# Kernel tuning notes

Measured on AMD Instinct MI355X. Metric: run time of the kernel, lower is better.

The kernel has to match this reference:

```python
import jax, jax.numpy as jnp
import numpy as np

B, S, D = 1, 2048, 1024
H, HD = 16, 64            # attn_num, head dim (D = H*HD)
TE, K, ED = 16, 2, 512    # experts, top_k, expert_dim
DS = 2048                 # shared_expert_dim
EPS = 1e-5
THETA = 10000.0
RSF = 1.0                 # routed_scaling_factor


def rmsnorm(x, w):
    return x * jax.lax.rsqrt(jnp.mean(x * x, axis=-1, keepdims=True) + EPS) * w


def rope(x):
    # x: [B,H,S,a]; half-split rotary as in RotaryEmb
    a = x.shape[-1]
    inv = (1.0 / THETA) ** (jnp.arange(0, a, 2, dtype=jnp.float32) / a)
    fr = jnp.outer(jnp.arange(x.shape[2], dtype=jnp.float32), inv)[None, None]  # [1,1,S,a/2]
    c, s = jnp.cos(fr), jnp.sin(fr)
    x1, x2 = jnp.split(x, 2, axis=-1)
    return jnp.concatenate([x1 * c + x2 * s, -x1 * s + x2 * c], axis=-1)


def setup_inputs() -> dict:
    key = jax.random.key(0)
    ks = jax.random.split(key, 16)
    w = 0.02
    return {
        "x_input": jax.random.normal(ks[0], (B, S, D), jnp.float32),
        "indices": jax.random.randint(ks[1], (B * S, K), 0, TE),
        "values": jax.random.normal(ks[2], (B * S, K), jnp.float32),
        "attn_w": jax.random.normal(ks[3], (3 * D, D), jnp.float32) * w,
        "attn_o_w": jax.random.normal(ks[4], (D, D), jnp.float32) * w,
        "attn_norm_w": jnp.ones((D,), jnp.float32),
        "ffn_norm_w": jnp.ones((D,), jnp.float32),
        "ffn_experts": jax.random.normal(ks[5], (3, TE, D, ED), jnp.float32) * w,
        "main_keys": jax.random.normal(ks[6], (D, TE), jnp.float32) * w,
        "main_bias": jnp.zeros((TE,), jnp.float32),
        "output_coeff": jnp.ones((1, 1, D), jnp.float32),
        "ffn_up_w": jax.random.normal(ks[7], (2 * DS, D), jnp.float32) * w,
        "ffn_down_w": jax.random.normal(ks[8], (D, DS), jnp.float32) * w,
        "shared_norm_w": jnp.ones((D,), jnp.float32),
    }


def reference(x_input, indices, values, attn_w, attn_o_w, attn_norm_w, ffn_norm_w,
              ffn_experts, main_keys, main_bias, output_coeff, ffn_up_w,
              ffn_down_w, shared_norm_w):
    # --- attention block ---
    x = rmsnorm(x_input, attn_norm_w)
    qkv = x @ attn_w.T                                  # [B,S,3D]
    xq, xk, xv = jnp.split(qkv, 3, axis=-1)
    def heads(t):
        return t.reshape(B, S, H, HD).transpose(0, 2, 1, 3)  # [B,H,S,HD]
    q, k, v = rope(heads(xq)), rope(heads(xk)), heads(xv)
    att = jnp.einsum('bhqa,bhka->bhqk', q, k) / jnp.sqrt(jnp.float32(HD))
    causal = jnp.tril(jnp.ones((S, S), bool))
    att = jnp.where(causal, att, jnp.finfo(att.dtype).min)
    att = jax.nn.softmax(att, axis=-1)
    o = jnp.einsum('bhqk,bhka->bhqa', att, v)
    x_attn = o.transpose(0, 2, 1, 3).reshape(B, S, D)
    x_ffn_input = x_attn @ attn_o_w.T + x_input

    # --- router ---
    x_ffn = rmsnorm(x_ffn_input, ffn_norm_w)
    T = B * S
    token_values = (x_ffn @ main_keys).reshape(T, TE)
    tv = jnp.take_along_axis(token_values, indices, axis=-1)  # [T,K]
    vals = values + tv + main_bias[indices]
    scores = jax.nn.softmax(vals, axis=-1) * RSF              # [T,K]

    # --- grouped GEMM experts (SwiGLU), dense combine over experts ---
    combine = jnp.zeros((T, TE), x_ffn.dtype).at[
        jnp.arange(T)[:, None], indices].add(scores)          # [T,TE]
    xf = x_ffn.reshape(T, D)
    h1 = jnp.einsum('td,edh->eth', xf, ffn_experts[0])
    h2 = jnp.einsum('td,edh->eth', xf, ffn_experts[1])
    g = jax.nn.silu(h1) * h2                                  # [TE,T,ED]
    ye = jnp.einsum('eth,edh->etd', g, ffn_experts[2])        # [TE,T,D]
    y = jnp.einsum('etd,te->td', ye, combine).reshape(B, S, D)
    y = y * output_coeff

    # --- shared SwiGLU expert ---
    x1, x2 = jnp.split(x_ffn @ ffn_up_w.T, 2, axis=-1)
    y_shared = (jax.nn.silu(x1) * x2) @ ffn_down_w.T
    y_shared = rmsnorm(y_shared, shared_norm_w)

    return y + y_shared + x_ffn_input
```

## Files before the change

### kernel.cpp

```cpp
#include <hip/hip_runtime.h>
#include <hip/hip_bf16.h>

using bf16 = __hip_bfloat16;

#define S_   2048
#define D_   1024
#define H_   16
#define HD_  64
#define TE_  16
#define ED_  512
#define DS_  2048
#define CAP_ 512

#define NEG_ -1e30f

typedef __attribute__((ext_vector_type(8))) short bf16x8;
typedef __attribute__((ext_vector_type(4))) short bf16x4;
typedef __attribute__((ext_vector_type(4))) float f32x4;
#define MFMA16(a, b, c) __builtin_amdgcn_mfma_f32_16x16x32_bf16(a, b, c, 0, 0, 0)

__device__ __forceinline__ void storeF(float* p, float v) { *p = v; }
__device__ __forceinline__ void storeF(bf16* p, float v)  { *p = __float2bfloat16(v); }
__device__ __forceinline__ short cvt1(float f) {
    bf16 h = __float2bfloat16(f);
    return *(short*)&h;
}
__device__ __forceinline__ float b2f(short s) {
    return __uint_as_float(((unsigned)(unsigned short)s) << 16);
}

__device__ __forceinline__ void load16(const bf16* g, short* l) {
    __builtin_amdgcn_global_load_lds(
        (const __attribute__((address_space(1))) unsigned*)g,
        (__attribute__((address_space(3))) unsigned*)l, 16, 0, 0);
}

__global__ __launch_bounds__(256) void convert_kernel(
        const float* __restrict__ src, bf16* __restrict__ dst)
{
    const size_t i = ((size_t)blockIdx.x*256 + threadIdx.x)*8;
    const float4 f0 = *(const float4*)(src + i);
    const float4 f1 = *(const float4*)(src + i + 4);
    short t8[8];
    t8[0]=cvt1(f0.x); t8[1]=cvt1(f0.y); t8[2]=cvt1(f0.z); t8[3]=cvt1(f0.w);
    t8[4]=cvt1(f1.x); t8[5]=cvt1(f1.y); t8[6]=cvt1(f1.z); t8[7]=cvt1(f1.w);
    *(bf16x8*)(dst + i) = *(bf16x8*)t8;
}

__global__ __launch_bounds__(256) void mkT_kernel(
        const float* __restrict__ mk, float* __restrict__ mkT)
{
    const int idx = blockIdx.x*256 + threadIdx.x;
    const int e = idx >> 10, d = idx & 1023;
    mkT[idx] = mk[d*TE_ + e];
}

__global__ __launch_bounds__(256) void rmsnorm_kernel(
        const float* __restrict__ x, const float* __restrict__ w,
        bf16* __restrict__ out)
{
    const int t = blockIdx.x, tid = threadIdx.x;
    __shared__ float red[4];
    const float4 xv = *(const float4*)(x + (size_t)t*D_ + tid*4);
    float ss = xv.x*xv.x + xv.y*xv.y + xv.z*xv.z + xv.w*xv.w;
#pragma unroll
    for (int off = 32; off; off >>= 1) ss += __shfl_xor(ss, off, 64);
    if ((tid & 63) == 0) red[tid >> 6] = ss;
    __syncthreads();
    const float rn = rsqrtf((red[0]+red[1]+red[2]+red[3]) * (1.f/D_) + 1e-5f);
    const float4 wv = *(const float4*)(w + tid*4);
    short o[4];
    o[0] = cvt1(xv.x*rn*wv.x); o[1] = cvt1(xv.y*rn*wv.y);
    o[2] = cvt1(xv.z*rn*wv.z); o[3] = cvt1(xv.w*rn*wv.w);
    *(bf16x4*)(out + (size_t)t*D_ + tid*4) = *(bf16x4*)o;
}

template<typename OutT, bool HAS_RES, int BN>
__global__ __launch_bounds__(256) void gemm_mfma_bb_kernel(
    const bf16* __restrict__ A, const bf16* __restrict__ B,
    OutT* __restrict__ C, const float* __restrict__ Res,
    int M, int N, int K)
{
    constexpr int MI = (BN == 128) ? 4 : 2;
    __shared__ short As[2][128*32];
    __shared__ short Bs[2][BN*32];
    const int tid = threadIdx.x;
    const int w = tid >> 6, l = tid & 63;
    const int wm = (BN == 128) ? (w >> 1) : w;
    const int wn = (BN == 128) ? (w & 1) : 0;
    const int nwg = gridDim.x * gridDim.y;
    const int bid = blockIdx.y * gridDim.x + blockIdx.x;
    const int swz = ((nwg & 7) == 0) ? ((bid & 7) * (nwg >> 3) + (bid >> 3)) : bid;
    const int bx = swz % gridDim.x, by = swz / gridDim.x;
    const int m0 = by * 128, n0 = bx * BN;
    const int lr = l >> 2, lq = l & 3;
    const int fm = l & 15, fq = l >> 4;
    f32x4 acc[MI][4];
#pragma unroll
    for (int i = 0; i < MI; ++i)
#pragma unroll
        for (int j = 0; j < 4; ++j) acc[i][j] = (f32x4){0.f,0.f,0.f,0.f};

    const bf16* ga = A + (size_t)(m0 + w*16 + lr)*K + lq*8;
    const bf16* gb = B + (size_t)(n0 + w*16 + lr)*K + lq*8;
    load16(ga,                &As[0][(w*16)*32]);
    load16(ga + (size_t)64*K, &As[0][(64 + w*16)*32]);
    load16(gb,                &Bs[0][(w*16)*32]);
    if constexpr (BN == 128)
        load16(gb + (size_t)64*K, &Bs[0][(64 + w*16)*32]);
    __syncthreads();
    const int nk = K >> 5;
    for (int t = 0; t < nk; ++t) {
        const int cur = t & 1;
        if (t + 1 < nk) {
            const int k1 = (t + 1) << 5;
            load16(ga + k1,                &As[cur^1][(w*16)*32]);
            load16(ga + k1 + (size_t)64*K, &As[cur^1][(64 + w*16)*32]);
            load16(gb + k1,                &Bs[cur^1][(w*16)*32]);
            if constexpr (BN == 128)
                load16(gb + k1 + (size_t)64*K, &Bs[cur^1][(64 + w*16)*32]);
        }
        bf16x8 af[MI], bfr[4];
#pragma unroll
        for (int mi = 0; mi < MI; ++mi)
            af[mi] = *(const bf16x8*)&As[cur][(wm*(MI*16) + mi*16 + fm)*32 + fq*8];
#pragma unroll
        for (int ni = 0; ni < 4; ++ni)
            bfr[ni] = *(const bf16x8*)&Bs[cur][(wn*64 + ni*16 + fm)*32 + fq*8];
#pragma unroll
        for (int mi = 0; mi < MI; ++mi)
#pragma unroll
            for (int ni = 0; ni < 4; ++ni)
                acc[mi][ni] = MFMA16(af[mi], bfr[ni], acc[mi][ni]);
        __syncthreads();
    }
#pragma unroll
    for (int mi = 0; mi < MI; ++mi)
#pragma unroll
        for (int ni = 0; ni < 4; ++ni)
#pragma unroll
            for (int r = 0; r < 4; ++r) {
                const int row = m0 + wm*(MI*16) + mi*16 + fq*4 + r;
                const int col = n0 + wn*64 + ni*16 + fm;
                float v = acc[mi][ni][r];
                if constexpr (HAS_RES) v += Res[(size_t)row*N + col];
                storeF(&C[(size_t)row*N + col], v);
            }
}

__global__ __launch_bounds__(256) void transpose_kernel(
    const float* __restrict__ src, bf16* __restrict__ dst)
{
    __shared__ bf16 tile[64][65];
    const int h0 = blockIdx.x*64, d0 = blockIdx.y*64, m = blockIdx.z;
    const float* s = src + (size_t)m*D_*ED_;
    bf16*        o = dst + (size_t)m*ED_*D_;
    const int tid = threadIdx.x;
#pragma unroll
    for (int i = 0; i < 16; ++i) {
        const int idx = tid + 256*i;
        const int r = idx >> 6, c = idx & 63;
        tile[r][c] = __float2bfloat16(s[(size_t)(d0 + r)*ED_ + h0 + c]);
    }
    __syncthreads();
#pragma unroll
    for (int i = 0; i < 16; ++i) {
        const int idx = tid + 256*i;
        const int r = idx >> 6, c = idx & 63;
        o[(size_t)(h0 + r)*D_ + d0 + c] = tile[c][r];
    }
}

__global__ __launch_bounds__(256) void expert_mid_mfma_kernel(
    const bf16* __restrict__ xffn, const bf16* __restrict__ w0t,
    const int* __restrict__ counts, const int* __restrict__ pairs,
    const float* __restrict__ pw, bf16* __restrict__ gbuf)
{
    const int ht = blockIdx.x, pt = blockIdx.y, e = blockIdx.z;
    const int cnt = counts[e];
    if (pt*128 >= cnt) return;
    __shared__ short Xs[2][128*32];
    __shared__ short W0s[2][64*32];
    __shared__ short W1s[2][64*32];
    __shared__ int   toks[128];
    __shared__ float wrow[128];
    const int tid = threadIdx.x;
    const int w = tid >> 6, l = tid & 63;
    const int wm = w >> 1, wn = w & 1;
    const int lr = l >> 2, lq = l & 3;
    const int fm = l & 15, fq = l >> 4;
    if (tid < 128) {
        const int p = pt*128 + tid;
        if (p < cnt) { toks[tid] = pairs[e*CAP_ + p] >> 1; wrow[tid] = pw[e*CAP_ + p]; }
        else         { toks[tid] = 0;                      wrow[tid] = 0.f; }
    }
    __syncthreads();
    const int t0 = toks[w*16 + lr], t1 = toks[64 + w*16 + lr];
    const bf16* gx0 = xffn + (size_t)t0*D_ + lq*8;
    const bf16* gx1 = xffn + (size_t)t1*D_ + lq*8;
    const bf16* g0  = w0t + ((size_t)e*ED_ + ht*64 + w*16 + lr)*D_ + lq*8;
    const bf16* g1  = w0t + ((size_t)(16 + e)*ED_ + ht*64 + w*16 + lr)*D_ + lq*8;
    f32x4 acc1[4][2], acc2[4][2];
#pragma unroll
    for (int i = 0; i < 4; ++i)
#pragma unroll
        for (int j = 0; j < 2; ++j) {
            acc1[i][j] = (f32x4){0.f,0.f,0.f,0.f};
            acc2[i][j] = (f32x4){0.f,0.f,0.f,0.f};
        }
    load16(gx0, &Xs[0][(w*16)*32]);
    load16(gx1, &Xs[0][(64 + w*16)*32]);
    load16(g0,  &W0s[0][(w*16)*32]);
    load16(g1,  &W1s[0][(w*16)*32]);
    __syncthreads();
    const int nk = D_ >> 5;
    for (int t = 0; t < nk; ++t) {
        const int cur = t & 1;
        if (t + 1 < nk) {
            const int k1 = (t + 1) << 5;
            load16(gx0 + k1, &Xs[cur^1][(w*16)*32]);
            load16(gx1 + k1, &Xs[cur^1][(64 + w*16)*32]);
            load16(g0 + k1,  &W0s[cur^1][(w*16)*32]);
            load16(g1 + k1,  &W1s[cur^1][(w*16)*32]);
        }
        bf16x8 af[4], b0[2], b1[2];
#pragma unroll
        for (int mi = 0; mi < 4; ++mi)
            af[mi] = *(const bf16x8*)&Xs[cur][(wm*64 + mi*16 + fm)*32 + fq*8];
#pragma unroll
        for (int ni = 0; ni < 2; ++ni) {
            b0[ni] = *(const bf16x8*)&W0s[cur][(wn*32 + ni*16 + fm)*32 + fq*8];
            b1[ni] = *(const bf16x8*)&W1s[cur][(wn*32 + ni*16 + fm)*32 + fq*8];
        }
#pragma unroll
        for (int mi = 0; mi < 4; ++mi)
#pragma unroll
            for (int ni = 0; ni < 2; ++ni) {
                acc1[mi][ni] = MFMA16(af[mi], b0[ni], acc1[mi][ni]);
                acc2[mi][ni] = MFMA16(af[mi], b1[ni], acc2[mi][ni]);
            }
        __syncthreads();
    }
#pragma unroll
    for (int mi = 0; mi < 4; ++mi)
#pragma unroll
        for (int ni = 0; ni < 2; ++ni)
#pragma unroll
            for (int r = 0; r < 4; ++r) {
                const int row = wm*64 + mi*16 + fq*4 + r;
                const int col = wn*32 + ni*16 + fm;
                const float h1 = acc1[mi][ni][r], h2 = acc2[mi][ni][r];
                const float g = wrow[row] * (h1 / (1.f + __expf(-h1))) * h2;
                gbuf[((size_t)e*CAP_ + pt*128 + row)*ED_ + ht*64 + col] = __float2bfloat16(g);
            }
}

__global__ __launch_bounds__(256) void expert_down_mfma_kernel(
    const bf16* __restrict__ gbuf, const bf16* __restrict__ w2,
    const int* __restrict__ counts, const int* __restrict__ pairs,
    bf16* __restrict__ ytk)
{
    const int nt = blockIdx.x, pt = blockIdx.y, e = blockIdx.z;
    const int cnt = counts[e];
    if (pt*128 >= cnt) return;
    __shared__ short As[2][128*32];
    __shared__ short Bs[2][128*32];
    __shared__ int prs[128];
    const int tid = threadIdx.x;
    const int w = tid >> 6, l = tid & 63;
    const int wm = w >> 1, wn = w & 1;
    const int lr = l >> 2, lq = l & 3;
    const int fm = l & 15, fq = l >> 4;
    if (tid < 128) {
        const int p = pt*128 + tid;
        prs[tid] = (p < cnt) ? pairs[e*CAP_ + p] : -1;
    }
    __syncthreads();
    const bf16* ga = gbuf + ((size_t)e*CAP_ + pt*128 + w*16 + lr)*ED_ + lq*8;
    const bf16* gb = w2 + (size_t)e*D_*ED_ + (size_t)(nt*128 + w*16 + lr)*ED_ + lq*8;
    f32x4 acc[4][4];
#pragma unroll
    for (int i = 0; i < 4; ++i)
#pragma unroll
        for (int j = 0; j < 4; ++j) acc[i][j] = (f32x4){0.f,0.f,0.f,0.f};
    load16(ga,                  &As[0][(w*16)*32]);
    load16(ga + (size_t)64*ED_, &As[0][(64 + w*16)*32]);
    load16(gb,                  &Bs[0][(w*16)*32]);
    load16(gb + (size_t)64*ED_, &Bs[0][(64 + w*16)*32]);
    __syncthreads();
    const int nk = ED_ >> 5;
    for (int t = 0; t < nk; ++t) {
        const int cur = t & 1;
        if (t + 1 < nk) {
            const int k1 = (t + 1) << 5;
            load16(ga + k1,                  &As[cur^1][(w*16)*32]);
            load16(ga + k1 + (size_t)64*ED_, &As[cur^1][(64 + w*16)*32]);
            load16(gb + k1,                  &Bs[cur^1][(w*16)*32]);
            load16(gb + k1 + (size_t)64*ED_, &Bs[cur^1][(64 + w*16)*32]);
        }
        bf16x8 af[4], bfr[4];
#pragma unroll
        for (int mi = 0; mi < 4; ++mi)
            af[mi] = *(const bf16x8*)&As[cur][(wm*64 + mi*16 + fm)*32 + fq*8];
#pragma unroll
        for (int ni = 0; ni < 4; ++ni)
            bfr[ni] = *(const bf16x8*)&Bs[cur][(wn*64 + ni*16 + fm)*32 + fq*8];
#pragma unroll
        for (int mi = 0; mi < 4; ++mi)
#pragma unroll
            for (int ni = 0; ni < 4; ++ni)
                acc[mi][ni] = MFMA16(af[mi], bfr[ni], acc[mi][ni]);
        __syncthreads();
    }
#pragma unroll
    for (int mi = 0; mi < 4; ++mi)
#pragma unroll
        for (int r = 0; r < 4; ++r) {
            const int pr = prs[wm*64 + mi*16 + fq*4 + r];
            if (pr < 0) continue;
#pragma unroll
            for (int ni = 0; ni < 4; ++ni) {
                const int col = nt*128 + wn*64 + ni*16 + fm;
                ytk[(size_t)pr*D_ + col] = __float2bfloat16(acc[mi][ni][r]);
            }
        }
}

__global__ __launch_bounds__(256) void rope_kernel(const bf16* __restrict__ qkv,
        bf16* __restrict__ qr, bf16* __restrict__ kswz)
{
    const int s = blockIdx.x, tid = threadIdx.x;
    const int c = s & 63, jt = s >> 6;
    for (int it = tid; it < 512; it += 256) {
        const int h = it >> 5, i = it & 31;
        const float inv = exp2f(-(float)i * 0.41524101186091903f);
        const float fr = (float)s * inv;
        float sn, cs;
        sincosf(fr, &sn, &cs);
        const size_t qb = (size_t)s*3072 + h*64 + i;
        const float q1 = __bfloat162float(qkv[qb]);
        const float q2 = __bfloat162float(qkv[qb + 32]);
        const size_t ob = ((size_t)h*S_ + s)*64 + i;
        qr[ob]      = __float2bfloat16(0.125f*( q1*cs + q2*sn));
        qr[ob + 32] = __float2bfloat16(0.125f*(-q1*sn + q2*cs));
        const float k1 = __bfloat162float(qkv[qb + 1024]);
        const float k2 = __bfloat162float(qkv[qb + 1024 + 32]);
        const size_t kb = ((size_t)(h*32 + jt))*4096 + (size_t)c*64;
        const int j0 = (i >> 3) ^ (c & 7);
        const int j1 = (4 + (i >> 3)) ^ (c & 7);
        kswz[kb + j0*8 + (i & 7)] = __float2bfloat16( k1*cs + k2*sn);
        kswz[kb + j1*8 + (i & 7)] = __float2bfloat16(-k1*sn + k2*cs);
    }
}

__global__ __launch_bounds__(256) void vtrans_kernel(
    const bf16* __restrict__ qkv, bf16* __restrict__ vswz)
{
    const int jt = blockIdx.x, h = blockIdx.y;
    __shared__ short Vt[64][72];
    const int tid = threadIdx.x;
#pragma unroll
    for (int it = 0; it < 2; ++it) {
        const int idx = it*256 + tid;
        const int cc = idx >> 3, seg = idx & 7;
        *(bf16x8*)&Vt[cc][seg*8] =
            *(const bf16x8*)(qkv + (size_t)(jt*64 + cc)*3072 + 2048 + h*64 + seg*8);
    }
    __syncthreads();
    bf16* out = vswz + ((size_t)(h*32 + jt))*4096;
#pragma unroll
    for (int it = 0; it < 2; ++it) {
        const int q = it*256 + tid;
        const int a = q >> 3, jo = q & 7;
        const int j = jo ^ (a & 7);
        short t8[8];
#pragma unroll
        for (int e = 0; e < 8; ++e) t8[e] = Vt[j*8 + e][a];
        *(bf16x8*)(out + a*64 + jo*8) = *(bf16x8*)t8;
    }
}

__global__ __launch_bounds__(512) void attn_mfma_kernel(
    const bf16* __restrict__ qr, const bf16* __restrict__ kswz,
    const bf16* __restrict__ vswz, bf16* __restrict__ xattn)
{
    const int p = blockIdx.x, h = blockIdx.y;
    __shared__ short Ks[2][2][4096];
    __shared__ short Vs[2][2][4096];
    __shared__ short Ps[2][64][72];
    __shared__ float Oc[64][64];
    __shared__ float Mc[64], Lc[64];
    const int tid = threadIdx.x;
    const int w = tid >> 6, l = tid & 63;
    const int g = w >> 2, gw = w & 3;
    const int fm = l & 15, fq = l >> 4;
    const int sr = gw * 16;
    const bf16* ktile = kswz + (size_t)h*32*4096;
    const bf16* vtile = vswz + (size_t)h*32*4096;

    auto stageKV = [&](int jtile, int bufidx) {
        const bf16* ks_ = ktile + (size_t)jtile*4096 + gw*1024 + l*8;
        const bf16* vs_ = vtile + (size_t)jtile*4096 + gw*1024 + l*8;
        short* kd_ = &Ks[g][bufidx][gw*1024];
        short* vd_ = &Vs[g][bufidx][gw*1024];
        load16(ks_,       kd_);
        load16(ks_ + 512, kd_ + 512);
        load16(vs_,       vd_);
        load16(vs_ + 512, vd_ + 512);
    };

    for (int half = 0; half < 2; ++half) {
        const int qt = half ? (31 - p) : p;
        const bf16* gq = qr + ((size_t)h*S_ + qt*64 + sr + fm)*64 + fq*8;
        const bf16x8 aq0 = *(const bf16x8*)gq;
        const bf16x8 aq1 = *(const bf16x8*)(gq + 32);
        f32x4 Oa[4];
        float m_i[4], l_i[4];
#pragma unroll
        for (int i = 0; i < 4; ++i) {
            Oa[i] = (f32x4){0.f,0.f,0.f,0.f};
            m_i[i] = NEG_; l_i[i] = 0.f;
        }
        const int nj = qt + 1;
        const int itmax = (nj + 1) >> 1;
        if (g < nj) stageKV(g, 0);
        __syncthreads();
        for (int it = 0; it < itmax; ++it) {
            const int jt = g + 2*it;
            const int buf = it & 1;
            if (jt + 2 < nj) stageKV(jt + 2, buf ^ 1);
            if (jt < nj) {
                const short* kb = &Ks[g][buf][0];
                const short* vb = &Vs[g][buf][0];
                f32x4 sc[4];
#pragma unroll
                for (int ni = 0; ni < 4; ++ni) sc[ni] = (f32x4){0.f,0.f,0.f,0.f};
                __builtin_amdgcn_s_setprio(1);
#pragma unroll
                for (int ni = 0; ni < 4; ++ni) {
                    const int row = ni*16 + fm;
                    bf16x8 bk0 = *(const bf16x8*)&kb[row*64 + (( fq      ^ (fm & 7))<<3)];
                    bf16x8 bk1 = *(const bf16x8*)&kb[row*64 + (((fq + 4) ^ (fm & 7))<<3)];
                    sc[ni] = MFMA16(aq0, bk0, sc[ni]);
                    sc[ni] = MFMA16(aq1, bk1, sc[ni]);
                }
                __builtin_amdgcn_s_setprio(0);
                const bool diag = (jt == qt);
#pragma unroll
                for (int r = 0; r < 4; ++r) {
                    const int rowin = sr + fq*4 + r;
                    float rm = NEG_;
#pragma unroll
                    for (int ni = 0; ni < 4; ++ni) {
                        if (diag && (ni*16 + fm) > rowin) sc[ni][r] = NEG_;
                        rm = fmaxf(rm, sc[ni][r]);
                    }
                    rm = fmaxf(rm, __shfl_xor(rm, 1, 16));
                    rm = fmaxf(rm, __shfl_xor(rm, 2, 16));
                    rm = fmaxf(rm, __shfl_xor(rm, 4, 16));
                    rm = fmaxf(rm, __shfl_xor(rm, 8, 16));
                    const float mnew  = fmaxf(m_i[r], rm);
                    const float alpha = __expf(m_i[r] - mnew);
                    float rs = 0.f;
#pragma unroll
                    for (int ni = 0; ni < 4; ++ni) {
                        const float pv = __expf(sc[ni][r] - mnew);
                        sc[ni][r] = pv; rs += pv;
                    }
                    rs += __shfl_xor(rs, 1, 16);
                    rs += __shfl_xor(rs, 2, 16);
                    rs += __shfl_xor(rs, 4, 16);
                    rs += __shfl_xor(rs, 8, 16);
                    l_i[r] = l_i[r]*alpha + rs;
                    m_i[r] = mnew;
#pragma unroll
                    for (int ni = 0; ni < 4; ++ni) Oa[ni][r] *= alpha;
                }
#pragma unroll
                for (int ni = 0; ni < 4; ++ni)
#pragma unroll
                    for (int r = 0; r < 4; ++r)
                        Ps[g][sr + fq*4 + r][ni*16 + fm] = cvt1(sc[ni][r]);
                bf16x8 ap0 = *(const bf16x8*)&Ps[g][sr + fm][fq*8];
                bf16x8 ap1 = *(const bf16x8*)&Ps[g][sr + fm][32 + fq*8];
                __builtin_amdgcn_s_setprio(1);
#pragma unroll
                for (int ni = 0; ni < 4; ++ni) {
                    const int row = ni*16 + fm;
                    bf16x8 bv0 = *(const bf16x8*)&vb[row*64 + (( fq      ^ (fm & 7))<<3)];
                    bf16x8 bv1 = *(const bf16x8*)&vb[row*64 + (((fq + 4) ^ (fm & 7))<<3)];
                    Oa[ni] = MFMA16(ap0, bv0, Oa[ni]);
                    Oa[ni] = MFMA16(ap1, bv1, Oa[ni]);
                }
                __builtin_amdgcn_s_setprio(0);
            }
            __syncthreads();
        }
        if (g == 1) {
#pragma unroll
            for (int r = 0; r < 4; ++r) {
                const int row = sr + fq*4 + r;
                if (fm == 0) { Mc[row] = m_i[r]; Lc[row] = l_i[r]; }
#pragma unroll
                for (int ni = 0; ni < 4; ++ni) Oc[row][ni*16 + fm] = Oa[ni][r];
            }
        }
        __syncthreads();
        if (g == 0) {
#pragma unroll
            for (int r = 0; r < 4; ++r) {
                const int row = sr + fq*4 + r;
                const float m1 = Mc[row], l1 = Lc[row];
                const float mm = fmaxf(m_i[r], m1);
                const float a0 = __expf(m_i[r] - mm), a1 = __expf(m1 - mm);
                const float inv = 1.f / (l_i[r]*a0 + l1*a1);
                const int srow = qt*64 + row;
#pragma unroll
                for (int ni = 0; ni < 4; ++ni)
                    xattn[(size_t)srow*D_ + h*64 + ni*16 + fm] =
                        __float2bfloat16((Oa[ni][r]*a0 + Oc[row][ni*16 + fm]*a1)*inv);
            }
        }
        __syncthreads();
    }
}

__global__ __launch_bounds__(256) void router_kernel(
    const bf16* __restrict__ xffn, const int* __restrict__ indices,
    const float* __restrict__ values, const float* __restrict__ mkT,
    const float* __restrict__ mbias, int* __restrict__ counts,
    int* __restrict__ pairs, float* __restrict__ pw)
{
    const int wv = threadIdx.x >> 6, lane = threadIdx.x & 63;
    const int t = blockIdx.x*4 + wv;
    const int i0 = indices[t*2], i1 = indices[t*2 + 1];
    const bf16* xp = xffn + (size_t)t*D_ + lane*16;
    const bf16x8 xa = *(const bf16x8*)xp;
    const bf16x8 xb = *(const bf16x8*)(xp + 8);
    float xv[16];
#pragma unroll
    for (int j = 0; j < 8; ++j) { xv[j] = b2f(xa[j]); xv[8 + j] = b2f(xb[j]); }
    const float* k0 = mkT + (size_t)i0*D_ + lane*16;
    const float* k1 = mkT + (size_t)i1*D_ + lane*16;
    float a0[16], a1[16];
#pragma unroll
    for (int j = 0; j < 4; ++j) {
        *(float4*)&a0[j*4] = *(const float4*)(k0 + j*4);
        *(float4*)&a1[j*4] = *(const float4*)(k1 + j*4);
    }
    float s0 = 0.f, s1 = 0.f;
#pragma unroll
    for (int j = 0; j < 16; ++j) {
        s0 = fmaf(xv[j], a0[j], s0);
        s1 = fmaf(xv[j], a1[j], s1);
    }
#pragma unroll
    for (int off = 32; off; off >>= 1) {
        s0 += __shfl_xor(s0, off, 64);
        s1 += __shfl_xor(s1, off, 64);
    }
    if (lane == 0) {
        const float v0 = values[t*2]     + s0 + mbias[i0];
        const float v1 = values[t*2 + 1] + s1 + mbias[i1];
        const float mx = fmaxf(v0, v1);
        const float e0 = __expf(v0 - mx), e1 = __expf(v1 - mx);
        const float inv = 1.f / (e0 + e1);
        const int p0 = atomicAdd(&counts[i0], 1);
        if (p0 < CAP_) { pairs[i0*CAP_ + p0] = t*2;     pw[i0*CAP_ + p0] = e0*inv; }
        const int p1 = atomicAdd(&counts[i1], 1);
        if (p1 < CAP_) { pairs[i1*CAP_ + p1] = t*2 + 1; pw[i1*CAP_ + p1] = e1*inv; }
    }
}

__global__ __launch_bounds__(256) void silu_mul_kernel(const bf16* __restrict__ u,
        bf16* __restrict__ gsh)
{
    const int idx = blockIdx.x*256 + threadIdx.x;
    const int t = idx >> 8, j = idx & 255;
    const bf16x8 av = *(const bf16x8*)(u + (size_t)t*(2*DS_) + j*8);
    const bf16x8 bv = *(const bf16x8*)(u + (size_t)t*(2*DS_) + DS_ + j*8);
    short o[8];
#pragma unroll
    for (int k = 0; k < 8; ++k) {
        const float a = b2f(av[k]), b = b2f(bv[k]);
        o[k] = cvt1(a / (1.f + __expf(-a)) * b);
    }
    *(bf16x8*)(gsh + (size_t)idx*8) = *(bf16x8*)o;
}

__global__ __launch_bounds__(256) void final_kernel(
    const bf16* __restrict__ ytk, const float* __restrict__ ysh,
    const float* __restrict__ xffin, const float* __restrict__ coeff,
    const float* __restrict__ shw, float* __restrict__ out)
{
    const int t = blockIdx.x, tid = threadIdx.x;
    __shared__ float red[4];
    const float4 yv = *(const float4*)(ysh + (size_t)t*D_ + tid*4);
    float ss = yv.x*yv.x + yv.y*yv.y + yv.z*yv.z + yv.w*yv.w;
#pragma unroll
    for (int off = 32; off; off >>= 1) ss += __shfl_xor(ss, off, 64);
    if ((tid & 63) == 0) red[tid >> 6] = ss;
    __syncthreads();
    const float rn = rsqrtf((red[0]+red[1]+red[2]+red[3]) * (1.f/D_) + 1e-5f);
    const int d = tid*4;
    const bf16x4 y0 = *(const bf16x4*)(ytk + (size_t)(t*2)*D_ + d);
    const bf16x4 y1 = *(const bf16x4*)(ytk + (size_t)(t*2 + 1)*D_ + d);
    const float4 cf = *(const float4*)(coeff + d);
    const float4 sw = *(const float4*)(shw + d);
    const float4 xf = *(const float4*)(xffin + (size_t)t*D_ + d);
    float4 o;
    o.x = (b2f(y0[0]) + b2f(y1[0]))*cf.x + yv.x*rn*sw.x + xf.x;
    o.y = (b2f(y0[1]) + b2f(y1[1]))*cf.y + yv.y*rn*sw.y + xf.y;
    o.z = (b2f(y0[2]) + b2f(y1[2]))*cf.z + yv.z*rn*sw.z + xf.z;
    o.w = (b2f(y0[3]) + b2f(y1[3]))*cf.w + yv.w*rn*sw.w + xf.w;
    *(float4*)(out + (size_t)t*D_ + d) = o;
}

extern "C" void kernel_launch(void* const* d_in, const int* in_sizes, int n_in,
                              void* d_out, int out_size, void* d_ws, size_t ws_size,
                              hipStream_t stream)
{
    const float* x_input     = (const float*)d_in[0];
    const int*   indices     = (const int*)  d_in[1];
    const float* values      = (const float*)d_in[2];
    const float* attn_w      = (const float*)d_in[3];
    const float* attn_o_w    = (const float*)d_in[4];
    const float* attn_norm_w = (const float*)d_in[5];
    const float* ffn_norm_w  = (const float*)d_in[6];
    const float* ffn_experts = (const float*)d_in[7];
    const float* main_keys   = (const float*)d_in[8];
    const float* main_bias   = (const float*)d_in[9];
    const float* out_coeff   = (const float*)d_in[10];
    const float* ffn_up_w    = (const float*)d_in[11];
    const float* ffn_down_w  = (const float*)d_in[12];
    const float* shared_nw   = (const float*)d_in[13];

    char* wp = (char*)d_ws;
    auto alloc = [&](size_t n) { char* p = wp; wp += (n + 255) & ~(size_t)255; return p; };
    char*  regA   = alloc(28*1024*1024 + 4096);
    bf16*  xn     = (bf16*)(regA);
    bf16*  qkv    = (bf16*)(regA + 4*1024*1024);
    bf16*  qr     = (bf16*)(regA + 16*1024*1024);
    bf16*  xattn  = (bf16*)(regA + 20*1024*1024);
    bf16*  w2bf   = (bf16*)(regA);
    bf16*  u      = (bf16*)(regA);
    bf16*  gsh    = (bf16*)(regA + 16*1024*1024);
    float* xffin  = (float*)alloc((size_t)S_*D_*4);
    bf16*  kswz   = (bf16*)xffin;
    bf16*  vswz   = kswz + (size_t)H_*32*4096;
    bf16*  xffn   = (bf16*) alloc((size_t)S_*D_*2);
    int*   counts = (int*)  alloc(TE_*4);
    int*   pairs  = (int*)  alloc((size_t)TE_*CAP_*4);
    float* pwgt   = (float*)alloc((size_t)TE_*CAP_*4);
    float* mkT    = (float*)alloc((size_t)TE_*D_*4);
    bf16*  gbuf   = (bf16*) alloc((size_t)TE_*CAP_*ED_*2);
    bf16*  o_bf   = (bf16*)gbuf;
    float* ysh    = (float*)((char*)gbuf);
    bf16*  ytk    = (bf16*) alloc((size_t)S_*2*D_*2);
    bf16*  awbf   = (bf16*)ytk;
    bf16*  w0t    = (bf16*) alloc((size_t)2*TE_*ED_*D_*2);
    bf16*  upbf   = (bf16*)w0t;
    bf16*  dnbf   = (bf16*)((char*)w0t + 8*1024*1024);

    hipMemsetAsync(counts, 0, TE_*4, stream);

    convert_kernel<<<(3*D_*D_)/2048, 256, 0, stream>>>(attn_w, awbf);
    convert_kernel<<<(D_*D_)/2048, 256, 0, stream>>>(attn_o_w, o_bf);
    mkT_kernel<<<(TE_*D_)/256, 256, 0, stream>>>(main_keys, mkT);

    rmsnorm_kernel<<<S_, 256, 0, stream>>>(x_input, attn_norm_w, xn);
    gemm_mfma_bb_kernel<bf16,false,128><<<dim3(3*D_/128, S_/128), 256, 0, stream>>>(
        xn, awbf, qkv, nullptr, S_, 3*D_, D_);
    rope_kernel<<<S_, 256, 0, stream>>>(qkv, qr, kswz);
    vtrans_kernel<<<dim3(S_/64, H_), 256, 0, stream>>>(qkv, vswz);
    attn_mfma_kernel<<<dim3(16, H_), 512, 0, stream>>>(qr, kswz, vswz, xattn);

    transpose_kernel<<<dim3(ED_/64, D_/64, 2*TE_), 256, 0, stream>>>(ffn_experts, w0t);

    gemm_mfma_bb_kernel<float,true,64><<<dim3(D_/64, S_/128), 256, 0, stream>>>(
        xattn, o_bf, xffin, x_input, S_, D_, D_);

    rmsnorm_kernel<<<S_, 256, 0, stream>>>(xffin, ffn_norm_w, xffn);
    router_kernel<<<S_/4, 256, 0, stream>>>(xffn, indices, values, mkT, main_bias,
                                            counts, pairs, pwgt);
    convert_kernel<<<(TE_*D_*ED_)/2048, 256, 0, stream>>>(
        ffn_experts + (size_t)2*TE_*D_*ED_, w2bf);
    expert_mid_mfma_kernel<<<dim3(ED_/64, CAP_/128, TE_), 256, 0, stream>>>(
        xffn, w0t, counts, pairs, pwgt, gbuf);
    convert_kernel<<<(2*DS_*D_)/2048, 256, 0, stream>>>(ffn_up_w, upbf);
    convert_kernel<<<(D_*DS_)/2048, 256, 0, stream>>>(ffn_down_w, dnbf);
    expert_down_mfma_kernel<<<dim3(D_/128, CAP_/128, TE_), 256, 0, stream>>>(
        gbuf, w2bf, counts, pairs, ytk);

    gemm_mfma_bb_kernel<bf16,false,128><<<dim3(2*DS_/128, S_/128), 256, 0, stream>>>(
        xffn, upbf, u, nullptr, S_, 2*DS_, D_);
    silu_mul_kernel<<<(S_*DS_)/2048, 256, 0, stream>>>(u, gsh);
    gemm_mfma_bb_kernel<float,false,64><<<dim3(D_/64, S_/128), 256, 0, stream>>>(
        gsh, dnbf, ysh, nullptr, S_, D_, DS_);

    final_kernel<<<S_, 256, 0, stream>>>(ytk, ysh, xffin, out_coeff, shared_nw,
                                         (float*)d_out);
}
```

Baseline: 494.3 us.

## Fuse shared-expert up GEMM with SwiGLU and vectorize expert weight transpose

Replaces the shared expert's up-projection GEMM followed by a separate silu_mul pass with one MFMA kernel. It computes the gate and up halves together and writes the SwiGLU result directly, so the 16MB intermediate never goes through memory and one launch disappears. The expert weight transpose kernel now reads float4 and writes 8-wide bf16 vectors instead of scalars. The fused kernel uses a 128x64 tile with two accumulator sets, which raises register pressure, and it is placed before the routed down-projection launch.

```diff
diff --git a/kernel.cpp b/kernel.cpp
--- a/kernel.cpp
+++ b/kernel.cpp
@@ -156,18 +156,25 @@
     const float* s = src + (size_t)m*D_*ED_;
     bf16*        o = dst + (size_t)m*ED_*D_;
     const int tid = threadIdx.x;
-#pragma unroll
-    for (int i = 0; i < 16; ++i) {
-        const int idx = tid + 256*i;
-        const int r = idx >> 6, c = idx & 63;
-        tile[r][c] = __float2bfloat16(s[(size_t)(d0 + r)*ED_ + h0 + c]);
-    }
-    __syncthreads();
-#pragma unroll
-    for (int i = 0; i < 16; ++i) {
-        const int idx = tid + 256*i;
-        const int r = idx >> 6, c = idx & 63;
-        o[(size_t)(h0 + r)*D_ + d0 + c] = tile[c][r];
+    const int r4 = tid >> 4, c4 = (tid & 15)*4;
+#pragma unroll
+    for (int i = 0; i < 4; ++i) {
+        const int r = i*16 + r4;
+        const float4 f = *(const float4*)&s[(size_t)(d0 + r)*ED_ + h0 + c4];
+        tile[r][c4+0] = __float2bfloat16(f.x);
+        tile[r][c4+1] = __float2bfloat16(f.y);
+        tile[r][c4+2] = __float2bfloat16(f.z);
+        tile[r][c4+3] = __float2bfloat16(f.w);
+    }
+    __syncthreads();
+    const int hh8 = tid >> 3, cg = tid & 7;
+#pragma unroll
+    for (int j = 0; j < 2; ++j) {
+        const int hh = j*32 + hh8;
+        short t8[8];
+#pragma unroll
+        for (int e = 0; e < 8; ++e) t8[e] = *(short*)&tile[cg*8 + e][hh];
+        *(bf16x8*)&o[(size_t)(h0 + hh)*D_ + d0 + cg*8] = *(bf16x8*)t8;
     }
 }
 
@@ -252,6 +259,79 @@
                 const float h1 = acc1[mi][ni][r], h2 = acc2[mi][ni][r];
                 const float g = wrow[row] * (h1 / (1.f + __expf(-h1))) * h2;
                 gbuf[((size_t)e*CAP_ + pt*128 + row)*ED_ + ht*64 + col] = __float2bfloat16(g);
+            }
+}
+
+__global__ __launch_bounds__(256) void shared_swiglu_kernel(
+    const bf16* __restrict__ xffn, const bf16* __restrict__ upbf,
+    bf16* __restrict__ gsh)
+{
+    const int nt = blockIdx.x, mt = blockIdx.y;
+    __shared__ short Xs[2][128*32];
+    __shared__ short W0s[2][64*32];
+    __shared__ short W1s[2][64*32];
+    const int tid = threadIdx.x;
+    const int w = tid >> 6, l = tid & 63;
+    const int wm = w >> 1, wn = w & 1;
+    const int lr = l >> 2, lq = l & 3;
+    const int fm = l & 15, fq = l >> 4;
+    const int m0 = mt*128, n0 = nt*64;
+    const bf16* gx0 = xffn + (size_t)(m0 + w*16 + lr)*D_ + lq*8;
+    const bf16* gx1 = xffn + (size_t)(m0 + 64 + w*16 + lr)*D_ + lq*8;
+    const bf16* g0  = upbf + (size_t)(n0 + w*16 + lr)*D_ + lq*8;
+    const bf16* g1  = upbf + (size_t)(DS_ + n0 + w*16 + lr)*D_ + lq*8;
+    f32x4 acc1[4][2], acc2[4][2];
+#pragma unroll
+    for (int i = 0; i < 4; ++i)
+#pragma unroll
+        for (int j = 0; j < 2; ++j) {
+            acc1[i][j] = (f32x4){0.f,0.f,0.f,0.f};
+            acc2[i][j] = (f32x4){0.f,0.f,0.f,0.f};
+        }
+    load16(gx0, &Xs[0][(w*16)*32]);
+    load16(gx1, &Xs[0][(64 + w*16)*32]);
+    load16(g0,  &W0s[0][(w*16)*32]);
+    load16(g1,  &W1s[0][(w*16)*32]);
+    __syncthreads();
+    const int nk = D_ >> 5;
+    for (int t = 0; t < nk; ++t) {
+        const int cur = t & 1;
+        if (t + 1 < nk) {
+            const int k1 = (t + 1) << 5;
+            load16(gx0 + k1, &Xs[cur^1][(w*16)*32]);
+            load16(gx1 + k1, &Xs[cur^1][(64 + w*16)*32]);
+            load16(g0 + k1,  &W0s[cur^1][(w*16)*32]);
+            load16(g1 + k1,  &W1s[cur^1][(w*16)*32]);
+        }
+        bf16x8 af[4], b0[2], b1[2];
+#pragma unroll
+        for (int mi = 0; mi < 4; ++mi)
+            af[mi] = *(const bf16x8*)&Xs[cur][(wm*64 + mi*16 + fm)*32 + fq*8];
+#pragma unroll
+        for (int ni = 0; ni < 2; ++ni) {
+            b0[ni] = *(const bf16x8*)&W0s[cur][(wn*32 + ni*16 + fm)*32 + fq*8];
+            b1[ni] = *(const bf16x8*)&W1s[cur][(wn*32 + ni*16 + fm)*32 + fq*8];
+        }
+#pragma unroll
+        for (int mi = 0; mi < 4; ++mi)
+#pragma unroll
+            for (int ni = 0; ni < 2; ++ni) {
+                acc1[mi][ni] = MFMA16(af[mi], b0[ni], acc1[mi][ni]);
+                acc2[mi][ni] = MFMA16(af[mi], b1[ni], acc2[mi][ni]);
+            }
+        __syncthreads();
+    }
+#pragma unroll
+    for (int mi = 0; mi < 4; ++mi)
+#pragma unroll
+        for (int ni = 0; ni < 2; ++ni)
+#pragma unroll
+            for (int r = 0; r < 4; ++r) {
+                const int row = wm*64 + mi*16 + fq*4 + r;
+                const int col = wn*32 + ni*16 + fm;
+                const float h1 = acc1[mi][ni][r], h2 = acc2[mi][ni][r];
+                const float g = (h1 / (1.f + __expf(-h1))) * h2;
+                gsh[(size_t)(m0 + row)*DS_ + n0 + col] = __float2bfloat16(g);
             }
 }
 
@@ -572,22 +652,6 @@
     }
 }
 
-__global__ __launch_bounds__(256) void silu_mul_kernel(const bf16* __restrict__ u,
-        bf16* __restrict__ gsh)
-{
-    const int idx = blockIdx.x*256 + threadIdx.x;
-    const int t = idx >> 8, j = idx & 255;
-    const bf16x8 av = *(const bf16x8*)(u + (size_t)t*(2*DS_) + j*8);
-    const bf16x8 bv = *(const bf16x8*)(u + (size_t)t*(2*DS_) + DS_ + j*8);
-    short o[8];
-#pragma unroll
-    for (int k = 0; k < 8; ++k) {
-        const float a = b2f(av[k]), b = b2f(bv[k]);
-        o[k] = cvt1(a / (1.f + __expf(-a)) * b);
-    }
-    *(bf16x8*)(gsh + (size_t)idx*8) = *(bf16x8*)o;
-}
-
 __global__ __launch_bounds__(256) void final_kernel(
     const bf16* __restrict__ ytk, const float* __restrict__ ysh,
     const float* __restrict__ xffin, const float* __restrict__ coeff,
@@ -643,7 +707,6 @@
     bf16*  qr     = (bf16*)(regA + 16*1024*1024);
     bf16*  xattn  = (bf16*)(regA + 20*1024*1024);
     bf16*  w2bf   = (bf16*)(regA);
-    bf16*  u      = (bf16*)(regA);
     bf16*  gsh    = (bf16*)(regA + 16*1024*1024);
     float* xffin  = (float*)alloc((size_t)S_*D_*4);
     bf16*  kswz   = (bf16*)xffin;
@@ -689,12 +752,12 @@
         xffn, w0t, counts, pairs, pwgt, gbuf);
     convert_kernel<<<(2*DS_*D_)/2048, 256, 0, stream>>>(ffn_up_w, upbf);
     convert_kernel<<<(D_*DS_)/2048, 256, 0, stream>>>(ffn_down_w, dnbf);
+
+    shared_swiglu_kernel<<<dim3(DS_/64, S_/128), 256, 0, stream>>>(xffn, upbf, gsh);
+
     expert_down_mfma_kernel<<<dim3(D_/128, CAP_/128, TE_), 256, 0, stream>>>(
         gbuf, w2bf, counts, pairs, ytk);
 
-    gemm_mfma_bb_kernel<bf16,false,128><<<dim3(2*DS_/128, S_/128), 256, 0, stream>>>(
-        xffn, upbf, u, nullptr, S_, 2*DS_, D_);
-    silu_mul_kernel<<<(S_*DS_)/2048, 256, 0, stream>>>(u, gsh);
     gemm_mfma_bb_kernel<float,false,64><<<dim3(D_/64, S_/128), 256, 0, stream>>>(
         gsh, dnbf, ysh, nullptr, S_, D_, DS_);
 
```

After: 489.6 us. Within noise of the previous version (-0.9%).
